# Performance work log

Hardware: AMD Instinct MI355X
Metric: run time of the kernel (lower is better)

## Reference

```python
import jax, jax.numpy as jnp
import numpy as np

# Sizes matching init_kwargs: r=2, J=3 -> K = 1 + (r-1)*J = 4 framelet operators
N, FEAT, K, NNZ = 20000, 64, 4, 320000
NU, GAMMA, J = 2.0, 1.0, 3  # nu, gamma_0 (gamma never updated on this code path)


def setup_inputs() -> dict:
    key = jax.random.key(0)
    ks = jax.random.split(key, 6)
    F = jax.random.normal(ks[0], (N, FEAT), dtype=jnp.float32)
    w_rows = jax.random.randint(ks[1], (K, NNZ), 0, N, dtype=jnp.int32)
    w_cols = jax.random.randint(ks[2], (K, NNZ), 0, N, dtype=jnp.int32)
    # scale ~1/avg_degree so the 14-step fixed-point iteration is contractive/stable
    w_vals = jax.random.normal(ks[3], (K, NNZ), dtype=jnp.float32) / 16.0
    d = jax.random.uniform(ks[4], (N,), dtype=jnp.float32)
    mask = jax.random.uniform(ks[5], (N, 1), dtype=jnp.float32)
    return {"F": F, "w_rows": w_rows, "w_cols": w_cols, "w_vals": w_vals,
            "d": d, "mask": mask, "thres_iter": 15}


def _spmm(rows, cols, vals, X):
    # sparse [N,N] @ dense [N,FEAT] via gather + segment-sum scatter
    return jax.ops.segment_sum(vals[:, None] * X[cols], rows, num_segments=N)


_spmm_shared = jax.vmap(_spmm, in_axes=(0, 0, 0, None))  # K operators, one dense X
_spmm_each = jax.vmap(_spmm, in_axes=(0, 0, 0, 0))       # K operators, K dense Xs


def _soft(x, thr):  # elementwise soft-thresholding: relu(x-t) - relu(-x-t)
    return jax.nn.relu(x - thr) - jax.nn.relu(-x - thr)


def reference(F, w_rows, w_cols, w_vals, d, mask, thres_iter):
    # nu_jl = [0] + [nu / 4^i for i in range(J)]
    nu = jnp.asarray([0.0] + [NU / (4.0 ** i) for i in range(J)], dtype=jnp.float32)  # [K]
    thr = (nu / GAMMA)[:, None, None] * d[None, :, None]  # [K,N,1] per-operator row thresholds
    d1 = d[:, None]                 # [N,1]
    m2 = mask * mask                # [N,1]
    denom = d1 * m2 + GAMMA         # [N,1]
    num_f = d1 * F * m2             # [N,FEAT]
    Y0 = jnp.zeros((K, N, FEAT), dtype=F.dtype)

    def step(carry, _):
        Uk, Y = carry
        # Z(k+1): soft-threshold of W_jl @ Uk + Y_jl / gamma
        Z = _soft(_spmm_shared(w_rows, w_cols, w_vals, Uk) + Y / GAMMA, thr)  # [K,N,FEAT]
        v = Y - GAMMA * Z
        WTV = _spmm_each(w_rows, w_cols, w_vals, v).sum(axis=0)               # [N,FEAT]
        Uk = (num_f - WTV) / denom
        # Y(k+1) dual update
        Y = Y + GAMMA * (_spmm_shared(w_rows, w_cols, w_vals, Uk) - Z)
        return (Uk, Y), None

    n_iter = int(thres_iter) - 1  # while k < thres_iter starting at k=1
    (Uk, _), _ = jax.lax.scan(jax.checkpoint(step), (F, Y0), None, length=n_iter)
    return Uk
```

## Files before the change

kernel.cpp:

```cpp
#include <hip/hip_runtime.h>


constexpr int N_    = 20000;
constexpr int FEAT_ = 64;
constexpr int K_    = 4;
constexpr int NNZ_  = 320000;
constexpr int NF    = N_ * FEAT_;
constexpr int KN    = K_ * N_;
constexpr int NEDGE = K_ * NNZ_;
constexpr int NITER = 14;
constexpr int BLK   = 256;
constexpr int NSB   = (KN + 255) / 256;
constexpr int NCPY  = 8;
constexpr int NXCD  = 8;
constexpr int EPV   = 2048;
constexpr int NVB   = NEDGE / EPV;

constexpr int T_SP  = 3;
constexpr int NW_SP = (N_ + T_SP - 1) / T_SP;
constexpr int NB_SP4 = (NW_SP + 3) / 4;
constexpr int TABSZ = 204;

constexpr int NB_WT4 = ((N_ / 4) + 3) / 4;
constexpr int WCAP  = 384;
constexpr int TABW  = WCAP + WCAP / 16;

constexpr int GB    = 6;

__constant__ float c_nu[4] = {0.0f, 2.0f, 0.5f, 0.125f};

__device__ __forceinline__ float softf(float x, float t) {
    float a = fabsf(x) - t;
    a = a > 0.0f ? a : 0.0f;
    return copysignf(a, x);
}

__device__ __forceinline__ float bf2f(unsigned short u) {
    union { unsigned int i; float f; } x;
    x.i = ((unsigned int)u) << 16;
    return x.f;
}
__device__ __forceinline__ unsigned short f2bf(float f) {
    union { float f; unsigned int i; } x;
    x.f = f;
    unsigned int r = x.i + 0x7FFFu + ((x.i >> 16) & 1u);
    return (unsigned short)(r >> 16);
}

__device__ __forceinline__ unsigned int val_bits(unsigned int p) {
    unsigned int e5 = (p >> 26) & 0x1Fu;
    unsigned int vb = (p & 0x80000000u) | ((e5 + 96u) << 23) |
                      (((p >> 17) & 0x1FFu) << 14);
    return (e5 == 0u) ? 0u : vb;
}

__device__ __forceinline__ unsigned long long enc_tab(unsigned int p) {
    unsigned int c16 = (p & 0x7FFFu) << 4;
    return ((unsigned long long)val_bits(p) << 32) | (unsigned long long)c16;
}

__device__ __forceinline__ unsigned long long enc_wtv(unsigned int p) {
    unsigned int c16 = (((p >> 15) & 3u) * (unsigned int)N_ +
                        (p & 0x7FFFu)) << 4;
    return ((unsigned long long)val_bits(p) << 32) | (unsigned long long)c16;
}

__device__ __forceinline__ void fma4(float4& acc, float v, const ushort4& x) {
    acc.x += v * bf2f(x.x);
    acc.y += v * bf2f(x.y);
    acc.z += v * bf2f(x.z);
    acc.w += v * bf2f(x.w);
}


__global__ __launch_bounds__(BLK) void precompute_kernel(
    const float* __restrict__ F, const float* __restrict__ d,
    const float* __restrict__ mask, float* __restrict__ dm,
    unsigned short* __restrict__ F_bf) {
    int i = blockIdx.x * BLK + threadIdx.x;
    if (i >= NF / 4) return;
    float4 f = ((const float4*)F)[i];
    ushort4 o;
    o.x = f2bf(f.x); o.y = f2bf(f.y); o.z = f2bf(f.z); o.w = f2bf(f.w);
    ((ushort4*)F_bf)[i] = o;
    if ((i & (FEAT_ / 4 - 1)) == 0) {
        int n = i / (FEAT_ / 4);
        dm[n] = d[n] * mask[n] * mask[n];
    }
}

__global__ __launch_bounds__(BLK) void hist_kernel(
    const int* __restrict__ rows, int* __restrict__ cnt8) {
    int e = blockIdx.x * BLK + threadIdx.x;
    if (e >= NEDGE) return;
    int k = e / NNZ_;
    int copy = blockIdx.x & (NCPY - 1);
    atomicAdd(&cnt8[copy * KN + rows[e] * K_ + k], 1);
}

__global__ __launch_bounds__(256) void scan1_kernel(
    const int* __restrict__ cnt8, int* __restrict__ loc,
    int* __restrict__ bsum) {
    int i = blockIdx.x * 256 + threadIdx.x;
    int x = 0;
    if (i < KN) {
        #pragma unroll
        for (int c = 0; c < NCPY; ++c) x += cnt8[c * KN + i];
    }
    int lane = threadIdx.x & 63, wid = threadIdx.x >> 6;
    int v = x;
    #pragma unroll
    for (int off = 1; off < 64; off <<= 1) {
        int t = __shfl_up(v, off, 64);
        if (lane >= off) v += t;
    }
    __shared__ int ws[4];
    if (lane == 63) ws[wid] = v;
    __syncthreads();
    int add = 0;
    for (int u = 0; u < wid; ++u) add += ws[u];
    v += add;
    if (i < KN) loc[i] = v - x;
    if (threadIdx.x == 255) bsum[blockIdx.x] = v;
}

__global__ __launch_bounds__(512) void scan2_kernel(int* __restrict__ bsum) {
    int tid = threadIdx.x;
    int x = (tid < NSB) ? bsum[tid] : 0;
    int lane = tid & 63, wid = tid >> 6;
    int v = x;
    #pragma unroll
    for (int off = 1; off < 64; off <<= 1) {
        int t = __shfl_up(v, off, 64);
        if (lane >= off) v += t;
    }
    __shared__ int ws[8];
    if (lane == 63) ws[wid] = v;
    __syncthreads();
    int add = 0;
    for (int u = 0; u < wid; ++u) add += ws[u];
    v += add;
    if (tid < NSB) bsum[tid] = v - x;
}

__global__ __launch_bounds__(256) void scan3_kernel(
    const int* __restrict__ loc, const int* __restrict__ bsum,
    int* __restrict__ offs, int* __restrict__ cursor) {
    int i = blockIdx.x * 256 + threadIdx.x;
    if (i < KN) {
        int v = loc[i] + bsum[blockIdx.x];
        offs[i] = v;
        cursor[i] = v;
    }
    if (i == 0) offs[KN] = NEDGE;
}

__global__ __launch_bounds__(BLK) void scatter_kernel(
    const int* __restrict__ rows, const int* __restrict__ cols,
    const float* __restrict__ vals, int* __restrict__ cursor,
    unsigned int* __restrict__ cmeta) {
    int xcd = blockIdx.x & (NXCD - 1);
    int vb  = blockIdx.x >> 3;
    int ebase = vb * EPV;
    #pragma unroll
    for (int i = 0; i < EPV / BLK; ++i) {
        int e = ebase + i * BLK + threadIdx.x;
        int row = rows[e];
        if (row / (N_ / NXCD) != xcd) continue;
        int k = e / NNZ_;
        unsigned int b  = __float_as_uint(vals[e]);
        unsigned int rb = b + 0x1FFFu + ((b >> 14) & 1u);
        int exp8 = (int)((rb >> 23) & 0xFF);
        unsigned int pk = 0u;
        if (exp8 > 96)
            pk = (b & 0x80000000u) | ((unsigned int)(exp8 - 96) << 26) |
                 (((rb >> 14) & 0x1FFu) << 17);
        pk |= ((unsigned int)k << 15) | (unsigned int)cols[e];
        int pos = atomicAdd(&cursor[row * K_ + k], 1);
        cmeta[pos] = pk;
    }
}


template <bool FIRST>
__global__ __launch_bounds__(BLK) void spmm_fused_kernel(
    const int* __restrict__ offs, const unsigned int* __restrict__ cmeta,
    const unsigned short* __restrict__ Xb,
    const float* __restrict__ d, unsigned short* __restrict__ V_bf) {
    __shared__ unsigned long long tab[4][2][TABSZ];
    int wave = (blockIdx.x * BLK + threadIdx.x) >> 6;
    int lane = threadIdx.x & 63;
    int sub  = lane >> 4, q = lane & 15;
    int widx = threadIdx.x >> 6;
    int n0 = wave * T_SP;
    if (n0 >= N_) return;
    int off_l = 0;
    if (lane <= 4 * T_SP) {
        int i = n0 * K_ + lane;
        if (i > KN) i = KN;
        off_l = offs[i];
    }
    const ushort4* X4 = (const ushort4*)Xb;
    ushort4* V4 = (ushort4*)V_bf;
    float nu_s = sub == 0 ? 0.0f : (sub == 1 ? 2.0f : (sub == 2 ? 0.5f : 0.125f));

    int tb = __shfl(off_l, 0, 64);
    int te = __shfl(off_l, 4, 64);
    int span = te - tb;
    unsigned int pA = 0, pB = 0, pC = 0;
    if (lane < span)       pA = cmeta[tb + lane];
    if (64 + lane < span)  pB = cmeta[tb + 64 + lane];
    if (128 + lane < span) pC = cmeta[tb + 128 + lane];

    #pragma unroll
    for (int t = 0; t < T_SP; ++t) {
        int n = n0 + t;
        if (n >= N_) break;
        unsigned long long* Tc = tab[widx][t & 1];
        int bs = __shfl(off_l, 4 * t + sub, 64);
        int es = __shfl(off_l, 4 * t + sub + 1, 64);
        int pre = bs - tb;
        int cnt = es - bs;
        int jmax = 192 - pre;
        jmax = cnt < jmax ? cnt : jmax;
        if (jmax < 0) jmax = 0;
        int maxc = jmax;
        { int o1 = __shfl_xor(maxc, 16, 64); maxc = maxc > o1 ? maxc : o1;
          int o2 = __shfl_xor(maxc, 32, 64); maxc = maxc > o2 ? maxc : o2; }
        if (lane < span)       { int s = lane;       Tc[s + (s >> 4)] = enc_tab(pA); }
        if (64 + lane < span)  { int s = 64 + lane;  Tc[s + (s >> 4)] = enc_tab(pB); }
        if (128 + lane < span) { int s = 128 + lane; Tc[s + (s >> 4)] = enc_tab(pC); }
        int tbn = te, ten = te, spann = 0;
        unsigned int nA = 0, nB = 0, nC = 0;
        if (t + 1 < T_SP && n + 1 < N_) {
            ten = __shfl(off_l, 4 * t + 8, 64);
            spann = ten - tbn;
            if (lane < spann)       nA = cmeta[tbn + lane];
            if (64 + lane < spann)  nB = cmeta[tbn + 64 + lane];
            if (128 + lane < spann) nC = cmeta[tbn + 128 + lane];
        }
        asm volatile("s_waitcnt lgkmcnt(0)" ::: "memory");
        float4 acc = {0.f, 0.f, 0.f, 0.f};
        for (int i0 = 0; i0 < maxc; i0 += GB) {
            float vv[GB]; int cc[GB];
            #pragma unroll
            for (int u = 0; u < GB; ++u) {
                int j = i0 + u;
                bool ok = j < jmax;
                int slot = ok ? pre + j : 0;
                unsigned long long e = Tc[slot + (slot >> 4)];
                cc[u] = (int)(unsigned int)e;
                vv[u] = ok ? __uint_as_float((unsigned int)(e >> 32)) : 0.0f;
            }
            ushort4 xx[GB];
            #pragma unroll
            for (int u = 0; u < GB; ++u) xx[u] = X4[cc[u] + q];
            #pragma unroll
            for (int u = 0; u < GB; ++u) fma4(acc, vv[u], xx[u]);
        }
        if (span > 192) {
            for (int e = tb + 192; e < te; ++e) {
                unsigned int p = cmeta[e];
                int ke = (int)((p >> 15) & 3u);
                unsigned long long en = enc_tab(p);
                if (sub == ke) {
                    ushort4 x = X4[(int)(unsigned int)en + q];
                    fma4(acc, __uint_as_float((unsigned int)(en >> 32)), x);
                }
            }
        }
        {
            float dn = d[n];
            int idx4 = (sub * N_ + n) * (FEAT_ / 4) + q;
            float thr = nu_s * dn;
            float4 y;
            if (FIRST) {
                y = make_float4(0.f, 0.f, 0.f, 0.f);
            } else {
                ushort4 vp = V4[idx4];
                y.x = acc.x + bf2f(vp.x); y.y = acc.y + bf2f(vp.y);
                y.z = acc.z + bf2f(vp.z); y.w = acc.w + bf2f(vp.w);
            }
            ushort4 o;
            o.x = f2bf(y.x - softf(acc.x + y.x, thr));
            o.y = f2bf(y.y - softf(acc.y + y.y, thr));
            o.z = f2bf(y.z - softf(acc.z + y.z, thr));
            o.w = f2bf(y.w - softf(acc.w + y.w, thr));
            V4[idx4] = o;
        }
        tb = tbn; te = ten; span = spann;
        pA = nA; pB = nB; pC = nC;
    }
}

template <bool LAST>
__global__ __launch_bounds__(BLK) void wtv_u_kernel(
    const int* __restrict__ offs, const unsigned int* __restrict__ cmeta,
    const unsigned short* __restrict__ V_bf,
    const float* __restrict__ F, const float* __restrict__ dm,
    float* __restrict__ U, unsigned short* __restrict__ U_bf) {
    __shared__ unsigned long long tab[4][TABW];
    int wave = (blockIdx.x * BLK + threadIdx.x) >> 6;
    int lane = threadIdx.x & 63;
    int sub  = lane >> 4, q = lane & 15;
    int widx = threadIdx.x >> 6;
    int n0 = wave * 4;
    if (n0 >= N_) return;
    int off_l = 0;
    if (lane <= 16) {
        int i = n0 * K_ + lane;
        if (i > KN) i = KN;
        off_l = offs[i];
    }
    const ushort4* V4 = (const ushort4*)V_bf;

    int tb = __shfl(off_l, 0, 64);
    int te = __shfl(off_l, 16, 64);
    int span = te - tb;
    unsigned int pr[6];
    #pragma unroll
    for (int c = 0; c < 6; ++c) {
        pr[c] = 0u;
        if (c * 64 + lane < span) pr[c] = cmeta[tb + c * 64 + lane];
    }
    int bs = __shfl(off_l, 4 * sub, 64);
    int es = __shfl(off_l, 4 * sub + 4, 64);
    int pre = bs - tb;
    int cnt = es - bs;
    int jmax = WCAP - pre;
    jmax = cnt < jmax ? cnt : jmax;
    if (jmax < 0) jmax = 0;
    int maxc = jmax;
    { int o1 = __shfl_xor(maxc, 16, 64); maxc = maxc > o1 ? maxc : o1;
      int o2 = __shfl_xor(maxc, 32, 64); maxc = maxc > o2 ? maxc : o2; }
    unsigned long long* Tc = tab[widx];
    #pragma unroll
    for (int c = 0; c < 6; ++c) {
        int s = c * 64 + lane;
        if (s < span) Tc[s + (s >> 4)] = enc_wtv(pr[c]);
    }
    asm volatile("s_waitcnt lgkmcnt(0)" ::: "memory");
    float4 acc = {0.f, 0.f, 0.f, 0.f};
    for (int i0 = 0; i0 < maxc; i0 += GB) {
        float vv[GB]; int cc[GB];
        #pragma unroll
        for (int u = 0; u < GB; ++u) {
            int j = i0 + u;
            bool ok = j < jmax;
            int slot = ok ? pre + j : 0;
            unsigned long long e = Tc[slot + (slot >> 4)];
            cc[u] = (int)(unsigned int)e;
            vv[u] = ok ? __uint_as_float((unsigned int)(e >> 32)) : 0.0f;
        }
        ushort4 xx[GB];
        #pragma unroll
        for (int u = 0; u < GB; ++u) xx[u] = V4[cc[u] + q];
        #pragma unroll
        for (int u = 0; u < GB; ++u) fma4(acc, vv[u], xx[u]);
    }
    if (span > WCAP) {
        for (int e = tb + WCAP; e < te; ++e) {
            unsigned int p = cmeta[e];
            unsigned long long en = enc_wtv(p);
            if (e >= bs && e < es) {
                ushort4 x = V4[(int)(unsigned int)en + q];
                fma4(acc, __uint_as_float((unsigned int)(en >> 32)), x);
            }
        }
    }
    {
        int n = n0 + sub;
        float dmv = dm[n];
        float r2 = 1.0f / (dmv + 1.0f);
        int idx4 = n * (FEAT_ / 4) + q;
        float4 f = ((const float4*)F)[idx4];
        float4 o;
        o.x = (dmv * f.x - acc.x) * r2; o.y = (dmv * f.y - acc.y) * r2;
        o.z = (dmv * f.z - acc.z) * r2; o.w = (dmv * f.w - acc.w) * r2;
        if (LAST) ((float4*)U)[idx4] = o;
        ushort4 ob;
        ob.x = f2bf(o.x); ob.y = f2bf(o.y);
        ob.z = f2bf(o.z); ob.w = f2bf(o.w);
        ((ushort4*)U_bf)[idx4] = ob;
    }
}

extern "C" void kernel_launch(void* const* d_in, const int* in_sizes, int n_in,
                              void* d_out, int out_size, void* d_ws, size_t ws_size,
                              hipStream_t stream) {
    const float* F      = (const float*)d_in[0];
    const int*   w_rows = (const int*)d_in[1];
    const int*   w_cols = (const int*)d_in[2];
    const float* w_vals = (const float*)d_in[3];
    const float* d      = (const float*)d_in[4];
    const float* mask   = (const float*)d_in[5];
    float* U = (float*)d_out;

    unsigned int* cmeta  = (unsigned int*)d_ws;
    unsigned short* V_bf = (unsigned short*)(cmeta + NEDGE);
    unsigned short* U_bf = V_bf + (size_t)KN * FEAT_;
    unsigned short* F_bf = U_bf + NF;
    float* dm     = (float*)(F_bf + NF);
    int*   cnt8   = (int*)(dm + N_);
    int*   loc    = cnt8 + NCPY * KN;
    int*   bsum   = loc + KN;
    int*   offs   = bsum + 512;
    int*   cursor = offs + KN + 1;

    const int gEdge = NEDGE / BLK;
    const int gNF4  = (NF / 4) / BLK;

    hipMemsetAsync(cnt8, 0, (size_t)NCPY * KN * 4, stream);
    precompute_kernel<<<gNF4, BLK, 0, stream>>>(F, d, mask, dm, F_bf);
    hist_kernel<<<gEdge, BLK, 0, stream>>>(w_rows, cnt8);
    scan1_kernel<<<NSB, 256, 0, stream>>>(cnt8, loc, bsum);
    scan2_kernel<<<1, 512, 0, stream>>>(bsum);
    scan3_kernel<<<NSB, 256, 0, stream>>>(loc, bsum, offs, cursor);
    scatter_kernel<<<NVB * NXCD, BLK, 0, stream>>>(w_rows, w_cols, w_vals,
                                                   cursor, cmeta);

    spmm_fused_kernel<true><<<NB_SP4, BLK, 0, stream>>>(offs, cmeta, F_bf, d, V_bf);
    for (int it = 0; it < NITER; ++it) {
        if (it < NITER - 1) {
            wtv_u_kernel<false><<<NB_WT4, BLK, 0, stream>>>(offs, cmeta, V_bf,
                                                            F, dm, U, U_bf);
            spmm_fused_kernel<false><<<NB_SP4, BLK, 0, stream>>>(offs, cmeta,
                                                                 U_bf, d, V_bf);
        } else {
            wtv_u_kernel<true><<<NB_WT4, BLK, 0, stream>>>(offs, cmeta, V_bf,
                                                           F, dm, U, U_bf);
        }
    }
}
```

Baseline: 780.4 us.

## Rebalance SpMM wave work: two rows per wave, split edge loop across half-waves

The transpose SpMM kernel now handles two rows per wave instead of four. Each row's edge list is split between two 16-lane groups, and their partial sums are combined with a cross-lane shuffle. The forward SpMM processes two rows per wave instead of three, the gather batch shrinks from 6 to 4, and both kernels get a launch-bounds occupancy hint of 8. The aim is more parallelism and shorter per-wave latency chains on the irregular gathers, at the cost of more waves, a shuffle reduction, and a smaller in-LDS cap (192) before the slow overflow path kicks in.

```diff
diff --git a/kernel.cpp b/kernel.cpp
--- a/kernel.cpp
+++ b/kernel.cpp
@@ -16,16 +16,18 @@
 constexpr int EPV   = 2048;
 constexpr int NVB   = NEDGE / EPV;
 
-constexpr int T_SP  = 3;
+constexpr int T_SP  = 2;
 constexpr int NW_SP = (N_ + T_SP - 1) / T_SP;
-constexpr int NB_SP4 = (NW_SP + 3) / 4;
-constexpr int TABSZ = 204;
-
-constexpr int NB_WT4 = ((N_ / 4) + 3) / 4;
-constexpr int WCAP  = 384;
+constexpr int NB_SP = (NW_SP + 3) / 4;
+constexpr int CAPS  = 192;
+constexpr int TABSZ = CAPS + CAPS / 16;
+
+constexpr int NW_WT = N_ / 2;
+constexpr int NB_WT = (NW_WT + 3) / 4;
+constexpr int WCAP  = 192;
 constexpr int TABW  = WCAP + WCAP / 16;
 
-constexpr int GB    = 6;
+constexpr int GB    = 4;
 
 __constant__ float c_nu[4] = {0.0f, 2.0f, 0.5f, 0.125f};
 
@@ -183,7 +185,7 @@
 
 
 template <bool FIRST>
-__global__ __launch_bounds__(BLK) void spmm_fused_kernel(
+__global__ __launch_bounds__(BLK, 8) void spmm_fused_kernel(
     const int* __restrict__ offs, const unsigned int* __restrict__ cmeta,
     const unsigned short* __restrict__ Xb,
     const float* __restrict__ d, unsigned short* __restrict__ V_bf) {
@@ -221,7 +223,7 @@
         int es = __shfl(off_l, 4 * t + sub + 1, 64);
         int pre = bs - tb;
         int cnt = es - bs;
-        int jmax = 192 - pre;
+        int jmax = CAPS - pre;
         jmax = cnt < jmax ? cnt : jmax;
         if (jmax < 0) jmax = 0;
         int maxc = jmax;
@@ -258,8 +260,8 @@
             #pragma unroll
             for (int u = 0; u < GB; ++u) fma4(acc, vv[u], xx[u]);
         }
-        if (span > 192) {
-            for (int e = tb + 192; e < te; ++e) {
+        if (span > CAPS) {
+            for (int e = tb + CAPS; e < te; ++e) {
                 unsigned int p = cmeta[e];
                 int ke = (int)((p >> 15) & 3u);
                 unsigned long long en = enc_tab(p);
@@ -294,7 +296,7 @@
 }
 
 template <bool LAST>
-__global__ __launch_bounds__(BLK) void wtv_u_kernel(
+__global__ __launch_bounds__(BLK, 8) void wtv_u_kernel(
     const int* __restrict__ offs, const unsigned int* __restrict__ cmeta,
     const unsigned short* __restrict__ V_bf,
     const float* __restrict__ F, const float* __restrict__ dm,
@@ -302,12 +304,14 @@
     __shared__ unsigned long long tab[4][TABW];
     int wave = (blockIdx.x * BLK + threadIdx.x) >> 6;
     int lane = threadIdx.x & 63;
-    int sub  = lane >> 4, q = lane & 15;
+    int half = lane >> 5;
+    int sub2 = (lane >> 4) & 1;
+    int q    = lane & 15;
     int widx = threadIdx.x >> 6;
-    int n0 = wave * 4;
+    int n0 = wave * 2;
     if (n0 >= N_) return;
     int off_l = 0;
-    if (lane <= 16) {
+    if (lane <= 8) {
         int i = n0 * K_ + lane;
         if (i > KN) i = KN;
         off_l = offs[i];
@@ -315,16 +319,14 @@
     const ushort4* V4 = (const ushort4*)V_bf;
 
     int tb = __shfl(off_l, 0, 64);
-    int te = __shfl(off_l, 16, 64);
+    int te = __shfl(off_l, 8, 64);
     int span = te - tb;
-    unsigned int pr[6];
-    #pragma unroll
-    for (int c = 0; c < 6; ++c) {
-        pr[c] = 0u;
-        if (c * 64 + lane < span) pr[c] = cmeta[tb + c * 64 + lane];
-    }
-    int bs = __shfl(off_l, 4 * sub, 64);
-    int es = __shfl(off_l, 4 * sub + 4, 64);
+    unsigned int p0 = 0u, p1 = 0u, p2 = 0u;
+    if (lane < span)       p0 = cmeta[tb + lane];
+    if (64 + lane < span)  p1 = cmeta[tb + 64 + lane];
+    if (128 + lane < span) p2 = cmeta[tb + 128 + lane];
+    int bs = __shfl(off_l, 4 * half, 64);
+    int es = __shfl(off_l, 4 * half + 4, 64);
     int pre = bs - tb;
     int cnt = es - bs;
     int jmax = WCAP - pre;
@@ -334,14 +336,12 @@
     { int o1 = __shfl_xor(maxc, 16, 64); maxc = maxc > o1 ? maxc : o1;
       int o2 = __shfl_xor(maxc, 32, 64); maxc = maxc > o2 ? maxc : o2; }
     unsigned long long* Tc = tab[widx];
-    #pragma unroll
-    for (int c = 0; c < 6; ++c) {
-        int s = c * 64 + lane;
-        if (s < span) Tc[s + (s >> 4)] = enc_wtv(pr[c]);
-    }
+    if (lane < span)       { int s = lane;       Tc[s + (s >> 4)] = enc_wtv(p0); }
+    if (64 + lane < span)  { int s = 64 + lane;  Tc[s + (s >> 4)] = enc_wtv(p1); }
+    if (128 + lane < span) { int s = 128 + lane; Tc[s + (s >> 4)] = enc_wtv(p2); }
     asm volatile("s_waitcnt lgkmcnt(0)" ::: "memory");
     float4 acc = {0.f, 0.f, 0.f, 0.f};
-    for (int i0 = 0; i0 < maxc; i0 += GB) {
+    for (int i0 = sub2 * GB; i0 < maxc; i0 += 2 * GB) {
         float vv[GB]; int cc[GB];
         #pragma unroll
         for (int u = 0; u < GB; ++u) {
@@ -358,6 +358,10 @@
         #pragma unroll
         for (int u = 0; u < GB; ++u) fma4(acc, vv[u], xx[u]);
     }
+    acc.x += __shfl_xor(acc.x, 16, 64);
+    acc.y += __shfl_xor(acc.y, 16, 64);
+    acc.z += __shfl_xor(acc.z, 16, 64);
+    acc.w += __shfl_xor(acc.w, 16, 64);
     if (span > WCAP) {
         for (int e = tb + WCAP; e < te; ++e) {
             unsigned int p = cmeta[e];
@@ -368,8 +372,8 @@
             }
         }
     }
-    {
-        int n = n0 + sub;
+    if (sub2 == 0) {
+        int n = n0 + half;
         float dmv = dm[n];
         float r2 = 1.0f / (dmv + 1.0f);
         int idx4 = n * (FEAT_ / 4) + q;
@@ -419,16 +423,16 @@
     scatter_kernel<<<NVB * NXCD, BLK, 0, stream>>>(w_rows, w_cols, w_vals,
                                                    cursor, cmeta);
 
-    spmm_fused_kernel<true><<<NB_SP4, BLK, 0, stream>>>(offs, cmeta, F_bf, d, V_bf);
+    spmm_fused_kernel<true><<<NB_SP, BLK, 0, stream>>>(offs, cmeta, F_bf, d, V_bf);
     for (int it = 0; it < NITER; ++it) {
         if (it < NITER - 1) {
-            wtv_u_kernel<false><<<NB_WT4, BLK, 0, stream>>>(offs, cmeta, V_bf,
-                                                            F, dm, U, U_bf);
-            spmm_fused_kernel<false><<<NB_SP4, BLK, 0, stream>>>(offs, cmeta,
-                                                                 U_bf, d, V_bf);
+            wtv_u_kernel<false><<<NB_WT, BLK, 0, stream>>>(offs, cmeta, V_bf,
+                                                           F, dm, U, U_bf);
+            spmm_fused_kernel<false><<<NB_SP, BLK, 0, stream>>>(offs, cmeta,
+                                                                U_bf, d, V_bf);
         } else {
-            wtv_u_kernel<true><<<NB_WT4, BLK, 0, stream>>>(offs, cmeta, V_bf,
-                                                           F, dm, U, U_bf);
-        }
-    }
-}
+            wtv_u_kernel<true><<<NB_WT, BLK, 0, stream>>>(offs, cmeta, V_bf,
+                                                          F, dm, U, U_bf);
+        }
+    }
+}
```

Result: slower. 802.3 us (+2.8%).
